# Performance work log

Measured on AMD Instinct MI355X. Metric: run time of the kernel, lower is better.

## Reference

```python
import jax, jax.numpy as jnp
import numpy as np

N, M, D, O = 16384, 4096, 256, 256

def setup_inputs() -> dict:
    key = jax.random.key(0)
    k1, k2, k3, k4, k5, k6, k7 = jax.random.split(key, 7)
    H_fine = jax.random.normal(k1, (N, D), dtype=jnp.float32)
    H_coarse = jax.random.normal(k2, (M, D), dtype=jnp.float32)
    inter_channel_adj = jax.random.randint(k3, (N, M), 0, 2).astype(jnp.float32)
    # attention = nn.Linear(2D, 1): weight vector [2D], bias scalar
    wa = jax.random.normal(k4, (2 * D,), dtype=jnp.float32) * (1.0 / np.sqrt(2 * D))
    ba = jax.random.normal(k5, (1,), dtype=jnp.float32) * 0.01
    # transform = nn.Linear(D, O), xavier_uniform weight
    lim = np.sqrt(6.0 / (D + O)).astype(np.float32)
    Wt = jax.random.uniform(k6, (O, D), minval=-lim, maxval=lim, dtype=jnp.float32)
    bt = jax.random.normal(k7, (O,), dtype=jnp.float32) * 0.01
    return {"H_fine": H_fine, "H_coarse": H_coarse,
            "inter_channel_adj": inter_channel_adj,
            "wa": wa, "ba": ba, "Wt": Wt, "bt": bt}

def reference(H_fine, H_coarse, inter_channel_adj, wa, ba, Wt, bt):
    d = H_fine.shape[-1]
    # additive attention: score_ij = [hf_i ; hc_j] . wa + b
    # = hf_i . wa[:d] + hc_j . wa[d:] + b  (avoids [N,M,2D] concat)
    sf = H_fine @ wa[:d]            # [N]
    sc = H_coarse @ wa[d:]          # [M]
    scores = sf[:, None] + sc[None, :] + ba[0]        # [N, M]
    masked = scores * inter_channel_adj               # [N, M]
    weights = jax.nn.softmax(masked, axis=-1)         # [N, M]
    attn_out = weights @ H_coarse                     # [N, D]
    attn_out = attn_out + H_fine                      # add_self=True
    out = attn_out @ Wt.T + bt                        # [N, O]
    return jax.nn.relu(out)
```

## Files before the change

### kernel.cpp

```cpp
#include <hip/hip_runtime.h>
#include <hip/hip_fp16.h>
#include <stdint.h>

#define N_ 16384
#define M_ 4096
#define D_ 256
#define O_ 256

#define WS_T    0
#define WS_U    65536
#define WS_R    81920
#define WS_WTP  98304
#define WS_BP   229376

typedef float  f32x4  __attribute__((ext_vector_type(4)));
typedef _Float16 half8 __attribute__((ext_vector_type(8)));

__device__ __forceinline__ unsigned short f2h(float f) {
  __half h = __float2half(f);
  unsigned short u;
  __builtin_memcpy(&u, &h, 2);
  return u;
}
__device__ __forceinline__ uint32_t hpack(float a, float b) {
  __half2 h = __floats2half2_rn(a, b);
  uint32_t u;
  __builtin_memcpy(&u, &h, 4);
  return u;
}

__global__ __launch_bounds__(256) void prep_kernel(
    const float* __restrict__ Hf, const float* __restrict__ Hc,
    const float* __restrict__ wa, const float* __restrict__ ba,
    const float* __restrict__ Wt, float* __restrict__ tv,
    float* __restrict__ uv, unsigned short* __restrict__ BP,
    unsigned short* __restrict__ WtP, float* __restrict__ Rv) {
  __shared__ float tile[64][65];
  __shared__ float red[4][64];
  int b = blockIdx.x;
  int t = threadIdx.x;
  if (b < 5120) {
    int wv = t >> 6, lane = t & 63;
    const float* X; const float* w; const float* bias; float* outv; int row;
    if (b < 4096) { X = Hf; w = wa;      bias = ba;      outv = tv; row = b * 4 + wv; }
    else          { X = Hc; w = wa + D_; bias = nullptr; outv = uv; row = (b - 4096) * 4 + wv; }
    const float4* x4 = (const float4*)(X + (size_t)row * D_);
    const float4* w4 = (const float4*)w;
    float4 xa = x4[lane], wa4 = w4[lane];
    float s = xa.x * wa4.x + xa.y * wa4.y + xa.z * wa4.z + xa.w * wa4.w;
#pragma unroll
    for (int off = 32; off > 0; off >>= 1) s += __shfl_xor(s, off);
    if (lane == 0) outv[row] = expf(s + (bias ? bias[0] : 0.0f));
  } else if (b < 5376) {
    int bb = b - 5120;
    int bk = bb >> 2;
    int bc = bb & 3;
    int k0 = bk * 64, col0 = bc * 64;
    int lane = t & 63, wv = t >> 6;
    int m = lane & 15, q = lane >> 4;
    float colsum = 0.0f;
#pragma unroll
    for (int i = 0; i < 16; ++i) {
      int e = t + 256 * i;
      int kk = e >> 6, cc = e & 63;
      float v = Hc[(size_t)(k0 + kk) * D_ + col0 + cc];
      tile[kk][cc] = v;
      colsum += v;
    }
    red[wv][t & 63] = colsum;
    __syncthreads();
    if (t < 64)
      atomicAdd(&Rv[col0 + t], red[0][t] + red[1][t] + red[2][t] + red[3][t]);
#pragma unroll
    for (int t8 = 0; t8 < 2; ++t8) {
      int tile_id = t8 * 4 + wv;
      int sub = tile_id >> 2, g = tile_id & 3;
      int kgg = bk * 2 + sub;
      int cgg = bc * 4 + g;
      unsigned short v8[8];
#pragma unroll
      for (int j = 0; j < 8; ++j)
        v8[j] = f2h(tile[sub * 32 + q * 8 + j][g * 16 + m]);
      *(uint4*)(BP + ((size_t)(kgg * 16 + cgg) * 64 + lane) * 8) = *(uint4*)v8;
    }
  } else {
    int tt = (b - 5376) * 256 + t;
    int lane = tt & 63, cg = (tt >> 6) & 15, kg = tt >> 10;
    int m = lane & 15, q = lane >> 4;
    const float* src = Wt + (size_t)(cg * 16 + m) * D_ + kg * 32 + q * 8;
    float4 w0 = *(const float4*)src, w1 = *(const float4*)(src + 4);
    unsigned short v8[8];
    v8[0] = f2h(w0.x); v8[1] = f2h(w0.y); v8[2] = f2h(w0.z); v8[3] = f2h(w0.w);
    v8[4] = f2h(w1.x); v8[5] = f2h(w1.y); v8[6] = f2h(w1.z); v8[7] = f2h(w1.w);
    *(uint4*)(WtP + (size_t)tt * 8) = *(uint4*)v8;
  }
}

__device__ __forceinline__ half8 frag_f16(uint32_t bits, __half2 th,
                                          const __half2* up, __half2 mone) {
  union { half8 h; uint32_t u[4]; } r;
#pragma unroll
  for (int p = 0; p < 4; ++p) {
    __half2 v = __hfma2(th, up[p], mone);
    uint32_t c;
    __builtin_memcpy(&c, &v, 4);
    uint32_t mlo = (uint32_t)((int32_t)(bits << (31 - 2 * p)) >> 31);
    uint32_t mhi = (uint32_t)((int32_t)(bits << (30 - 2 * p)) >> 31);
    r.u[p] = c & ((mlo & 0x0000FFFFu) | (mhi & 0xFFFF0000u));
  }
  return r.h;
}

__global__ __launch_bounds__(1024, 4) void mega_kernel(
    const float* __restrict__ adj, const unsigned short* __restrict__ BP,
    const float* __restrict__ tv, const float* __restrict__ uv,
    const float* __restrict__ Rv, const float* __restrict__ Hf,
    const unsigned short* __restrict__ WtP, const float* __restrict__ bt,
    float* __restrict__ out) {
  __shared__ __align__(16) char smem[123648];
  unsigned int (*bt2)[130] = (unsigned int (*)[130])(smem);
  float* u_lds = (float*)(smem + 33280);
  uint32_t* u_h2 = (uint32_t*)(smem + 49664);
  float (*Cred)[256] = (float (*)[256])(smem + 57856);
  float* Lsum_lds = (float*)(smem + 123392);
  unsigned short (*attn)[264] = (unsigned short (*)[264])(smem);

  int tid = threadIdx.x;
  int w = tid >> 6, lane = tid & 63;
  int q = lane >> 4, m = lane & 15;
  int colq = w >> 2, ksub = w & 3;
  int i0 = blockIdx.x * 64;

  for (int i = tid; i < M_ / 2; i += 1024) {
    float2 u2 = *(const float2*)(uv + 2 * i);
    u_lds[2 * i] = u2.x; u_lds[2 * i + 1] = u2.y;
    u_h2[i] = hpack(u2.x, u2.y);
  }
  __syncthreads();

#pragma unroll 1
  for (int pass = 0; pass < 2; ++pass) {
    int r0 = w * 4 + pass * 2;
    const float* arA = adj + ((size_t)i0 + r0) * M_;
    const float* arB = arA + M_;
    float suA = 0.f, scA = 0.f, suB = 0.f, scB = 0.f;
    float a0 = arA[lane], a1 = arA[64 + lane], a2 = arA[128 + lane], a3 = arA[192 + lane];
    float b0 = arB[lane], b1 = arB[64 + lane], b2 = arB[128 + lane], b3 = arB[192 + lane];
#pragma unroll 1
    for (int i = 0; i < 16; ++i) {
      int k0 = i * 256;
      int k1 = (i + 1 < 16) ? k0 + 256 : 0;
      float na0 = arA[k1 + lane],       na1 = arA[k1 + 64 + lane];
      float na2 = arA[k1 + 128 + lane], na3 = arA[k1 + 192 + lane];
      float nb0 = arB[k1 + lane],       nb1 = arB[k1 + 64 + lane];
      float nb2 = arB[k1 + 128 + lane], nb3 = arB[k1 + 192 + lane];

      unsigned long long wA0 = __ballot(a0 != 0.0f), wA1 = __ballot(a1 != 0.0f);
      unsigned long long wA2 = __ballot(a2 != 0.0f), wA3 = __ballot(a3 != 0.0f);
      unsigned long long wB0 = __ballot(b0 != 0.0f), wB1 = __ballot(b1 != 0.0f);
      unsigned long long wB2 = __ballot(b2 != 0.0f), wB3 = __ballot(b3 != 0.0f);
      suA = fmaf(a0, u_lds[k0 + lane], suA);
      suA = fmaf(a1, u_lds[k0 + 64 + lane], suA);
      suA = fmaf(a2, u_lds[k0 + 128 + lane], suA);
      suA = fmaf(a3, u_lds[k0 + 192 + lane], suA);
      scA += (a0 + a1) + (a2 + a3);
      suB = fmaf(b0, u_lds[k0 + lane], suB);
      suB = fmaf(b1, u_lds[k0 + 64 + lane], suB);
      suB = fmaf(b2, u_lds[k0 + 128 + lane], suB);
      suB = fmaf(b3, u_lds[k0 + 192 + lane], suB);
      scB += (b0 + b1) + (b2 + b3);
      if (lane < 16) {
        int rowsel = lane >> 3;
        int c = (lane >> 1) & 3, hi = lane & 1;
        unsigned long long v = rowsel ? (c == 0 ? wB0 : c == 1 ? wB1 : c == 2 ? wB2 : wB3)
                                      : (c == 0 ? wA0 : c == 1 ? wA1 : c == 2 ? wA2 : wA3);
        bt2[r0 + rowsel][i * 8 + c * 2 + hi] =
            hi ? (unsigned int)(v >> 32) : (unsigned int)v;
      }
      a0 = na0; a1 = na1; a2 = na2; a3 = na3;
      b0 = nb0; b1 = nb1; b2 = nb2; b3 = nb3;
    }
#pragma unroll
    for (int off = 32; off > 0; off >>= 1) {
      suA += __shfl_xor(suA, off); scA += __shfl_xor(scA, off);
      suB += __shfl_xor(suB, off); scB += __shfl_xor(scB, off);
    }
    if (lane == 0) {
      Lsum_lds[r0]     = tv[i0 + r0] * suA - scA;
      Lsum_lds[r0 + 1] = tv[i0 + r0 + 1] * suB - scB;
    }
  }

  const unsigned short* bbase = BP + (size_t)(colq * 4) * 512 + (size_t)lane * 8;
  int kg0 = ksub * 32;
  half8 bufA[4], bufB[4];
#pragma unroll
  for (int n = 0; n < 4; ++n)
    bufA[n] = *(const half8*)(bbase + ((size_t)kg0 * 16 + n) * 512);

  __half2 th0 = __float2half2_rn(tv[i0 + m]);
  __half2 th1 = __float2half2_rn(tv[i0 + 16 + m]);
  __half2 th2 = __float2half2_rn(tv[i0 + 32 + m]);
  __half2 th3 = __float2half2_rn(tv[i0 + 48 + m]);
  const __half2 mone = __float2half2_rn(-1.0f);

  f32x4 acc[4][4];
#pragma unroll
  for (int s = 0; s < 4; ++s)
#pragma unroll
    for (int n = 0; n < 4; ++n) acc[s][n] = (f32x4){0.f, 0.f, 0.f, 0.f};

  __syncthreads();

#pragma unroll 1
  for (int it2 = 0; it2 < 16; ++it2) {
    int kg = kg0 + it2 * 2;
    uint2 W0 = *(const uint2*)&bt2[m][kg];
    uint2 W1 = *(const uint2*)&bt2[16 + m][kg];
    uint2 W2 = *(const uint2*)&bt2[32 + m][kg];
    uint2 W3 = *(const uint2*)&bt2[48 + m][kg];
    int sh = q * 8;

#pragma unroll
    for (int n = 0; n < 4; ++n)
      bufB[n] = *(const half8*)(bbase + ((size_t)(kg + 1) * 16 + n) * 512);
    {
      uint4 uu = *(const uint4*)&u_h2[kg * 16 + q * 4];
      __half2 up[4];
      __builtin_memcpy(up, &uu, 16);
      half8 af;
      af = frag_f16((W0.x >> sh) & 0xffu, th0, up, mone);
#pragma unroll
      for (int n = 0; n < 4; ++n)
        acc[0][n] = __builtin_amdgcn_mfma_f32_16x16x32_f16(af, bufA[n], acc[0][n], 0, 0, 0);
      af = frag_f16((W1.x >> sh) & 0xffu, th1, up, mone);
#pragma unroll
      for (int n = 0; n < 4; ++n)
        acc[1][n] = __builtin_amdgcn_mfma_f32_16x16x32_f16(af, bufA[n], acc[1][n], 0, 0, 0);
      af = frag_f16((W2.x >> sh) & 0xffu, th2, up, mone);
#pragma unroll
      for (int n = 0; n < 4; ++n)
        acc[2][n] = __builtin_amdgcn_mfma_f32_16x16x32_f16(af, bufA[n], acc[2][n], 0, 0, 0);
      af = frag_f16((W3.x >> sh) & 0xffu, th3, up, mone);
#pragma unroll
      for (int n = 0; n < 4; ++n)
        acc[3][n] = __builtin_amdgcn_mfma_f32_16x16x32_f16(af, bufA[n], acc[3][n], 0, 0, 0);
    }

    int kn = (it2 + 1 < 16) ? kg + 2 : kg0;
#pragma unroll
    for (int n = 0; n < 4; ++n)
      bufA[n] = *(const half8*)(bbase + ((size_t)kn * 16 + n) * 512);
    {
      uint4 uu = *(const uint4*)&u_h2[(kg + 1) * 16 + q * 4];
      __half2 up[4];
      __builtin_memcpy(up, &uu, 16);
      half8 af;
      af = frag_f16((W0.y >> sh) & 0xffu, th0, up, mone);
#pragma unroll
      for (int n = 0; n < 4; ++n)
        acc[0][n] = __builtin_amdgcn_mfma_f32_16x16x32_f16(af, bufB[n], acc[0][n], 0, 0, 0);
      af = frag_f16((W1.y >> sh) & 0xffu, th1, up, mone);
#pragma unroll
      for (int n = 0; n < 4; ++n)
        acc[1][n] = __builtin_amdgcn_mfma_f32_16x16x32_f16(af, bufB[n], acc[1][n], 0, 0, 0);
      af = frag_f16((W2.y >> sh) & 0xffu, th2, up, mone);
#pragma unroll
      for (int n = 0; n < 4; ++n)
        acc[2][n] = __builtin_amdgcn_mfma_f32_16x16x32_f16(af, bufB[n], acc[2][n], 0, 0, 0);
      af = frag_f16((W3.y >> sh) & 0xffu, th3, up, mone);
#pragma unroll
      for (int n = 0; n < 4; ++n)
        acc[3][n] = __builtin_amdgcn_mfma_f32_16x16x32_f16(af, bufB[n], acc[3][n], 0, 0, 0);
    }
  }

#pragma unroll
  for (int s4 = 0; s4 < 4; ++s4) {
    if (ksub == s4) {
#pragma unroll
      for (int s = 0; s < 4; ++s)
#pragma unroll
        for (int n = 0; n < 4; ++n) {
          int col = colq * 64 + n * 16 + m;
#pragma unroll
          for (int r = 0; r < 4; ++r) {
            int rl = s * 16 + q * 4 + r;
            if (s4 == 0) Cred[rl][col] = acc[s][n][r];
            else         Cred[rl][col] += acc[s][n][r];
          }
        }
    }
    __syncthreads();
  }

  {
    int row = tid >> 4;
    int c0 = (tid & 15) * 16;
    size_t grow = (size_t)i0 + row;
    float invL = 1.0f / (Lsum_lds[row] + (float)M_);
    const float* hfp = Hf + grow * D_ + c0;
    const float* rvp = Rv + c0;
    const float* crp = &Cred[row][c0];
#pragma unroll
    for (int g = 0; g < 4; ++g) {
      float4 cv = *(const float4*)(crp + g * 4);
      float4 rv = *(const float4*)(rvp + g * 4);
      float4 hv = *(const float4*)(hfp + g * 4);
      float v0 = fmaf(cv.x + rv.x, invL, hv.x);
      float v1 = fmaf(cv.y + rv.y, invL, hv.y);
      float v2 = fmaf(cv.z + rv.z, invL, hv.z);
      float v3 = fmaf(cv.w + rv.w, invL, hv.w);
      *(uint32_t*)&attn[row][c0 + g * 4]     = hpack(v0, v1);
      *(uint32_t*)&attn[row][c0 + g * 4 + 2] = hpack(v2, v3);
    }
  }
  __syncthreads();

  {
    int rt = w & 3, cq = w >> 2;
    f32x4 facc[4];
#pragma unroll
    for (int n = 0; n < 4; ++n) facc[n] = (f32x4){0.f, 0.f, 0.f, 0.f};
    const unsigned short* wwave = WtP + (size_t)(cq * 4) * 512 + (size_t)lane * 8;
#pragma unroll
    for (int kf = 0; kf < 8; ++kf) {
      half8 af = *(const half8*)&attn[rt * 16 + m][kf * 32 + q * 8];
#pragma unroll
      for (int n = 0; n < 4; ++n) {
        half8 bf = *(const half8*)(wwave + ((size_t)kf * 16 + n) * 512);
        facc[n] = __builtin_amdgcn_mfma_f32_16x16x32_f16(af, bf, facc[n], 0, 0, 0);
      }
    }
#pragma unroll
    for (int n = 0; n < 4; ++n) {
      int col = cq * 64 + n * 16 + m;
      float b = bt[col];
#pragma unroll
      for (int r = 0; r < 4; ++r) {
        size_t row = (size_t)i0 + rt * 16 + q * 4 + r;
        out[row * O_ + col] = fmaxf(facc[n][r] + b, 0.0f);
      }
    }
  }
}

extern "C" void kernel_launch(void* const* d_in, const int* in_sizes, int n_in,
                              void* d_out, int out_size, void* d_ws, size_t ws_size,
                              hipStream_t stream) {
  const float* Hf  = (const float*)d_in[0];
  const float* Hc  = (const float*)d_in[1];
  const float* adj = (const float*)d_in[2];
  const float* wa  = (const float*)d_in[3];
  const float* ba  = (const float*)d_in[4];
  const float* Wt  = (const float*)d_in[5];
  const float* bt  = (const float*)d_in[6];
  float* out = (float*)d_out;

  char* ws = (char*)d_ws;
  float* tv   = (float*)(ws + WS_T);
  float* uv   = (float*)(ws + WS_U);
  float* Rv   = (float*)(ws + WS_R);
  unsigned short* WtP = (unsigned short*)(ws + WS_WTP);
  unsigned short* BP  = (unsigned short*)(ws + WS_BP);

  hipMemsetAsync(Rv, 0, D_ * sizeof(float), stream);

  prep_kernel<<<5408, 256, 0, stream>>>(Hf, Hc, wa, ba, Wt, tv, uv, BP, WtP, Rv);
  mega_kernel<<<256, 1024, 0, stream>>>(adj, BP, tv, uv, Rv, Hf, WtP, bt, out);
}
```

Measured before the change: 440.8 us.

## Halve block row tile to 32 rows with 512 threads and 512 blocks

Result: no change. 441.5 us (+0.1%).

```diff
diff --git a/kernel.cpp b/kernel.cpp
--- a/kernel.cpp
+++ b/kernel.cpp
@@ -111,88 +111,110 @@
   return r.h;
 }
 
-__global__ __launch_bounds__(1024, 4) void mega_kernel(
+#define COMPUTE_K(WB0, WB1, KK, BUF)                                          \
+  {                                                                           \
+    uint4 uu = *(const uint4*)&u_h2[(KK) * 16 + q * 4];                       \
+    __half2 up[4];                                                            \
+    __builtin_memcpy(up, &uu, 16);                                            \
+    half8 af = frag_f16(((WB0) >> sh) & 0xffu, th0, up, mone);                \
+    _Pragma("unroll")                                                         \
+    for (int n = 0; n < 4; ++n)                                               \
+      acc[0][n] = __builtin_amdgcn_mfma_f32_16x16x32_f16(af, BUF[n], acc[0][n], 0, 0, 0); \
+    af = frag_f16(((WB1) >> sh) & 0xffu, th1, up, mone);                      \
+    _Pragma("unroll")                                                         \
+    for (int n = 0; n < 4; ++n)                                               \
+      acc[1][n] = __builtin_amdgcn_mfma_f32_16x16x32_f16(af, BUF[n], acc[1][n], 0, 0, 0); \
+  }
+
+__global__ __launch_bounds__(512, 4) void mega_kernel(
     const float* __restrict__ adj, const unsigned short* __restrict__ BP,
     const float* __restrict__ tv, const float* __restrict__ uv,
     const float* __restrict__ Rv, const float* __restrict__ Hf,
     const unsigned short* __restrict__ WtP, const float* __restrict__ bt,
     float* __restrict__ out) {
-  __shared__ __align__(16) char smem[123648];
-  unsigned int (*bt2)[130] = (unsigned int (*)[130])(smem);
-  float* u_lds = (float*)(smem + 33280);
-  uint32_t* u_h2 = (uint32_t*)(smem + 49664);
-  float (*Cred)[256] = (float (*)[256])(smem + 57856);
-  float* Lsum_lds = (float*)(smem + 123392);
+  __shared__ __align__(16) char smem[74880];
+  unsigned int (*bt2)[132] = (unsigned int (*)[132])(smem);
+  float* u_lds = (float*)(smem + 16896);
+  uint32_t* u_h2 = (uint32_t*)(smem + 33280);
+  float (*Cred)[260] = (float (*)[260])(smem + 41472);
+  float* Lsum_lds = (float*)(smem + 74752);
   unsigned short (*attn)[264] = (unsigned short (*)[264])(smem);
 
   int tid = threadIdx.x;
   int w = tid >> 6, lane = tid & 63;
   int q = lane >> 4, m = lane & 15;
-  int colq = w >> 2, ksub = w & 3;
-  int i0 = blockIdx.x * 64;
-
-  for (int i = tid; i < M_ / 2; i += 1024) {
+  int colq = w >> 1, ksub = w & 1;
+  int i0 = blockIdx.x * 32;
+
+  for (int i = tid; i < M_ / 2; i += 512) {
     float2 u2 = *(const float2*)(uv + 2 * i);
     u_lds[2 * i] = u2.x; u_lds[2 * i + 1] = u2.y;
     u_h2[i] = hpack(u2.x, u2.y);
   }
   __syncthreads();
 
-#pragma unroll 1
-  for (int pass = 0; pass < 2; ++pass) {
-    int r0 = w * 4 + pass * 2;
-    const float* arA = adj + ((size_t)i0 + r0) * M_;
-    const float* arB = arA + M_;
-    float suA = 0.f, scA = 0.f, suB = 0.f, scB = 0.f;
-    float a0 = arA[lane], a1 = arA[64 + lane], a2 = arA[128 + lane], a3 = arA[192 + lane];
-    float b0 = arB[lane], b1 = arB[64 + lane], b2 = arB[128 + lane], b3 = arB[192 + lane];
+  {
+    int r0 = w * 4;
+    const float* ar = adj + ((size_t)i0 + r0) * M_;
+    float su[4] = {0.f, 0.f, 0.f, 0.f}, sc[4] = {0.f, 0.f, 0.f, 0.f};
+    float a[4][4], na[4][4];
+#pragma unroll
+    for (int j = 0; j < 4; ++j)
+#pragma unroll
+      for (int c = 0; c < 4; ++c)
+        a[j][c] = ar[(size_t)j * M_ + c * 64 + lane];
 #pragma unroll 1
     for (int i = 0; i < 16; ++i) {
       int k0 = i * 256;
       int k1 = (i + 1 < 16) ? k0 + 256 : 0;
-      float na0 = arA[k1 + lane],       na1 = arA[k1 + 64 + lane];
-      float na2 = arA[k1 + 128 + lane], na3 = arA[k1 + 192 + lane];
-      float nb0 = arB[k1 + lane],       nb1 = arB[k1 + 64 + lane];
-      float nb2 = arB[k1 + 128 + lane], nb3 = arB[k1 + 192 + lane];
-
-      unsigned long long wA0 = __ballot(a0 != 0.0f), wA1 = __ballot(a1 != 0.0f);
-      unsigned long long wA2 = __ballot(a2 != 0.0f), wA3 = __ballot(a3 != 0.0f);
-      unsigned long long wB0 = __ballot(b0 != 0.0f), wB1 = __ballot(b1 != 0.0f);
-      unsigned long long wB2 = __ballot(b2 != 0.0f), wB3 = __ballot(b3 != 0.0f);
-      suA = fmaf(a0, u_lds[k0 + lane], suA);
-      suA = fmaf(a1, u_lds[k0 + 64 + lane], suA);
-      suA = fmaf(a2, u_lds[k0 + 128 + lane], suA);
-      suA = fmaf(a3, u_lds[k0 + 192 + lane], suA);
-      scA += (a0 + a1) + (a2 + a3);
-      suB = fmaf(b0, u_lds[k0 + lane], suB);
-      suB = fmaf(b1, u_lds[k0 + 64 + lane], suB);
-      suB = fmaf(b2, u_lds[k0 + 128 + lane], suB);
-      suB = fmaf(b3, u_lds[k0 + 192 + lane], suB);
-      scB += (b0 + b1) + (b2 + b3);
-      if (lane < 16) {
+#pragma unroll
+      for (int j = 0; j < 4; ++j)
+#pragma unroll
+        for (int c = 0; c < 4; ++c)
+          na[j][c] = ar[(size_t)j * M_ + k1 + c * 64 + lane];
+      unsigned long long bal[4][4];
+#pragma unroll
+      for (int j = 0; j < 4; ++j) {
+#pragma unroll
+        for (int c = 0; c < 4; ++c) {
+          bal[j][c] = __ballot(a[j][c] != 0.0f);
+          su[j] = fmaf(a[j][c], u_lds[k0 + c * 64 + lane], su[j]);
+        }
+        sc[j] += (a[j][0] + a[j][1]) + (a[j][2] + a[j][3]);
+      }
+      if (lane < 32) {
         int rowsel = lane >> 3;
         int c = (lane >> 1) & 3, hi = lane & 1;
-        unsigned long long v = rowsel ? (c == 0 ? wB0 : c == 1 ? wB1 : c == 2 ? wB2 : wB3)
-                                      : (c == 0 ? wA0 : c == 1 ? wA1 : c == 2 ? wA2 : wA3);
+        unsigned long long v0 = (c == 0) ? bal[0][0] : (c == 1) ? bal[0][1] : (c == 2) ? bal[0][2] : bal[0][3];
+        unsigned long long v1 = (c == 0) ? bal[1][0] : (c == 1) ? bal[1][1] : (c == 2) ? bal[1][2] : bal[1][3];
+        unsigned long long v2 = (c == 0) ? bal[2][0] : (c == 1) ? bal[2][1] : (c == 2) ? bal[2][2] : bal[2][3];
+        unsigned long long v3 = (c == 0) ? bal[3][0] : (c == 1) ? bal[3][1] : (c == 2) ? bal[3][2] : bal[3][3];
+        unsigned long long v = (rowsel == 0) ? v0 : (rowsel == 1) ? v1 : (rowsel == 2) ? v2 : v3;
         bt2[r0 + rowsel][i * 8 + c * 2 + hi] =
             hi ? (unsigned int)(v >> 32) : (unsigned int)v;
       }
-      a0 = na0; a1 = na1; a2 = na2; a3 = na3;
-      b0 = nb0; b1 = nb1; b2 = nb2; b3 = nb3;
+#pragma unroll
+      for (int j = 0; j < 4; ++j)
+#pragma unroll
+        for (int c = 0; c < 4; ++c) a[j][c] = na[j][c];
     }
 #pragma unroll
     for (int off = 32; off > 0; off >>= 1) {
-      suA += __shfl_xor(suA, off); scA += __shfl_xor(scA, off);
-      suB += __shfl_xor(suB, off); scB += __shfl_xor(scB, off);
+#pragma unroll
+      for (int j = 0; j < 4; ++j) {
+        su[j] += __shfl_xor(su[j], off);
+        sc[j] += __shfl_xor(sc[j], off);
+      }
     }
     if (lane == 0) {
-      Lsum_lds[r0]     = tv[i0 + r0] * suA - scA;
-      Lsum_lds[r0 + 1] = tv[i0 + r0 + 1] * suB - scB;
+#pragma unroll
+      for (int j = 0; j < 4; ++j)
+        Lsum_lds[r0 + j] = tv[i0 + r0 + j] * su[j] - sc[j];
     }
   }
 
   const unsigned short* bbase = BP + (size_t)(colq * 4) * 512 + (size_t)lane * 8;
-  int kg0 = ksub * 32;
+  int kg0 = ksub * 64;
   half8 bufA[4], bufB[4];
 #pragma unroll
   for (int n = 0; n < 4; ++n)
@@ -200,86 +222,40 @@
 
   __half2 th0 = __float2half2_rn(tv[i0 + m]);
   __half2 th1 = __float2half2_rn(tv[i0 + 16 + m]);
-  __half2 th2 = __float2half2_rn(tv[i0 + 32 + m]);
-  __half2 th3 = __float2half2_rn(tv[i0 + 48 + m]);
   const __half2 mone = __float2half2_rn(-1.0f);
 
-  f32x4 acc[4][4];
-#pragma unroll
-  for (int s = 0; s < 4; ++s)
+  f32x4 acc[2][4];
+#pragma unroll
+  for (int s = 0; s < 2; ++s)
 #pragma unroll
     for (int n = 0; n < 4; ++n) acc[s][n] = (f32x4){0.f, 0.f, 0.f, 0.f};
 
   __syncthreads();
 
 #pragma unroll 1
-  for (int it2 = 0; it2 < 16; ++it2) {
+  for (int it2 = 0; it2 < 32; ++it2) {
     int kg = kg0 + it2 * 2;
     uint2 W0 = *(const uint2*)&bt2[m][kg];
     uint2 W1 = *(const uint2*)&bt2[16 + m][kg];
-    uint2 W2 = *(const uint2*)&bt2[32 + m][kg];
-    uint2 W3 = *(const uint2*)&bt2[48 + m][kg];
     int sh = q * 8;
 
 #pragma unroll
     for (int n = 0; n < 4; ++n)
       bufB[n] = *(const half8*)(bbase + ((size_t)(kg + 1) * 16 + n) * 512);
-    {
-      uint4 uu = *(const uint4*)&u_h2[kg * 16 + q * 4];
-      __half2 up[4];
-      __builtin_memcpy(up, &uu, 16);
-      half8 af;
-      af = frag_f16((W0.x >> sh) & 0xffu, th0, up, mone);
-#pragma unroll
-      for (int n = 0; n < 4; ++n)
-        acc[0][n] = __builtin_amdgcn_mfma_f32_16x16x32_f16(af, bufA[n], acc[0][n], 0, 0, 0);
-      af = frag_f16((W1.x >> sh) & 0xffu, th1, up, mone);
-#pragma unroll
-      for (int n = 0; n < 4; ++n)
-        acc[1][n] = __builtin_amdgcn_mfma_f32_16x16x32_f16(af, bufA[n], acc[1][n], 0, 0, 0);
-      af = frag_f16((W2.x >> sh) & 0xffu, th2, up, mone);
-#pragma unroll
-      for (int n = 0; n < 4; ++n)
-        acc[2][n] = __builtin_amdgcn_mfma_f32_16x16x32_f16(af, bufA[n], acc[2][n], 0, 0, 0);
-      af = frag_f16((W3.x >> sh) & 0xffu, th3, up, mone);
-#pragma unroll
-      for (int n = 0; n < 4; ++n)
-        acc[3][n] = __builtin_amdgcn_mfma_f32_16x16x32_f16(af, bufA[n], acc[3][n], 0, 0, 0);
-    }
-
-    int kn = (it2 + 1 < 16) ? kg + 2 : kg0;
+    COMPUTE_K(W0.x, W1.x, kg, bufA)
+
+    int kn = (it2 + 1 < 32) ? kg + 2 : kg0;
 #pragma unroll
     for (int n = 0; n < 4; ++n)
       bufA[n] = *(const half8*)(bbase + ((size_t)kn * 16 + n) * 512);
-    {
-      uint4 uu = *(const uint4*)&u_h2[(kg + 1) * 16 + q * 4];
-      __half2 up[4];
-      __builtin_memcpy(up, &uu, 16);
-      half8 af;
-      af = frag_f16((W0.y >> sh) & 0xffu, th0, up, mone);
-#pragma unroll
-      for (int n = 0; n < 4; ++n)
-        acc[0][n] = __builtin_amdgcn_mfma_f32_16x16x32_f16(af, bufB[n], acc[0][n], 0, 0, 0);
-      af = frag_f16((W1.y >> sh) & 0xffu, th1, up, mone);
-#pragma unroll
-      for (int n = 0; n < 4; ++n)
-        acc[1][n] = __builtin_amdgcn_mfma_f32_16x16x32_f16(af, bufB[n], acc[1][n], 0, 0, 0);
-      af = frag_f16((W2.y >> sh) & 0xffu, th2, up, mone);
-#pragma unroll
-      for (int n = 0; n < 4; ++n)
-        acc[2][n] = __builtin_amdgcn_mfma_f32_16x16x32_f16(af, bufB[n], acc[2][n], 0, 0, 0);
-      af = frag_f16((W3.y >> sh) & 0xffu, th3, up, mone);
-#pragma unroll
-      for (int n = 0; n < 4; ++n)
-        acc[3][n] = __builtin_amdgcn_mfma_f32_16x16x32_f16(af, bufB[n], acc[3][n], 0, 0, 0);
-    }
-  }
-
-#pragma unroll
-  for (int s4 = 0; s4 < 4; ++s4) {
+    COMPUTE_K(W0.y, W1.y, kg + 1, bufB)
+  }
+
+#pragma unroll
+  for (int s4 = 0; s4 < 2; ++s4) {
     if (ksub == s4) {
 #pragma unroll
-      for (int s = 0; s < 4; ++s)
+      for (int s = 0; s < 2; ++s)
 #pragma unroll
         for (int n = 0; n < 4; ++n) {
           int col = colq * 64 + n * 16 + m;
@@ -318,7 +294,7 @@
   __syncthreads();
 
   {
-    int rt = w & 3, cq = w >> 2;
+    int rt = w & 1, cq = w >> 1;
     f32x4 facc[4];
 #pragma unroll
     for (int n = 0; n < 4; ++n) facc[n] = (f32x4){0.f, 0.f, 0.f, 0.f};
@@ -367,5 +343,5 @@
   hipMemsetAsync(Rv, 0, D_ * sizeof(float), stream);
 
   prep_kernel<<<5408, 256, 0, stream>>>(Hf, Hc, wa, ba, Wt, tv, uv, BP, WtP, Rv);
-  mega_kernel<<<256, 1024, 0, stream>>>(adj, BP, tv, uv, Rv, Hf, WtP, bt, out);
-}
+  mega_kernel<<<512, 512, 0, stream>>>(adj, BP, tv, uv, Rv, Hf, WtP, bt, out);
+}
```
